# Optimization experiments

Measured on AMD Instinct MI355X. Metric: run time of the kernel, lower is better.

Reference implementation:

```python
import jax, jax.numpy as jnp
import numpy as np

N = 50000
E = 800000
HIGH, LOW, EMB = 128, 32, 64
HID, HEADS, OUT = 32, 8, 8
IN1 = HIGH + EMB  # 192
IN2 = HID * HEADS  # 256
NEG_SLOPE = 0.2


def setup_inputs() -> dict:
    key = jax.random.key(0)
    ks = jax.random.split(key, 12)
    s = lambda k, shape: (jax.random.normal(k, shape, dtype=jnp.float32) * 0.1)
    return {
        "high_dim_features": jax.random.normal(ks[0], (N, HIGH), dtype=jnp.float32),
        "low_dim_features": jax.random.normal(ks[1], (N, LOW), dtype=jnp.float32),
        "edge_index": jax.random.randint(ks[2], (2, E), 0, N, dtype=jnp.int32),
        "W_emb": s(ks[3], (LOW, EMB)),
        "b_emb": jnp.zeros((EMB,), jnp.float32),
        "W1": s(ks[4], (IN1, HEADS * HID)),
        "att_src1": s(ks[5], (HEADS, HID)),
        "att_dst1": s(ks[6], (HEADS, HID)),
        "b1": jnp.zeros((HEADS * HID,), jnp.float32),
        "W2": s(ks[7], (IN2, OUT)),
        "att_src2": s(ks[8], (1, OUT)),
        "att_dst2": s(ks[9], (1, OUT)),
        "b2": jnp.zeros((OUT,), jnp.float32),
    }


def _gat_layer(x, src, dst, W, att_src, att_dst, bias, heads, out_ch, concat):
    # x: [N, F_in]; src/dst: [E'] (self-loops already appended)
    n = x.shape[0]
    h = (x @ W).reshape(n, heads, out_ch)            # [N, H, C]
    a_src = jnp.einsum('nhc,hc->nh', h, att_src)     # [N, H]
    a_dst = jnp.einsum('nhc,hc->nh', h, att_dst)
    alpha = a_src[src] + a_dst[dst]                  # [E', H]
    alpha = jax.nn.leaky_relu(alpha, NEG_SLOPE)
    # segment softmax over incoming edges per destination node
    m = jax.ops.segment_max(alpha, dst, num_segments=n)
    ea = jnp.exp(alpha - m[dst])
    z = jax.ops.segment_sum(ea, dst, num_segments=n)
    alpha = ea / (z[dst] + 1e-16)                    # [E', H]
    msg = h[src] * alpha[:, :, None]                 # [E', H, C]
    out = jax.ops.segment_sum(msg, dst, num_segments=n)  # [N, H, C]
    if concat:
        out = out.reshape(n, heads * out_ch)
    else:
        out = out.mean(axis=1)
    return out + bias


def reference(high_dim_features, low_dim_features, edge_index,
              W_emb, b_emb, W1, att_src1, att_dst1, b1,
              W2, att_src2, att_dst2, b2):
    # embedding + elu, concat
    emb = jax.nn.elu(low_dim_features @ W_emb + b_emb)
    x = jnp.concatenate([high_dim_features, emb], axis=1)  # [N, IN1]
    # add self-loops (PyG default)
    loops = jnp.arange(N, dtype=edge_index.dtype)
    src = jnp.concatenate([edge_index[0], loops])
    dst = jnp.concatenate([edge_index[1], loops])
    x = _gat_layer(x, src, dst, W1, att_src1, att_dst1, b1, HEADS, HID, True)
    x = jax.nn.elu(x)  # dropout: eval mode no-op
    x = _gat_layer(x, src, dst, W2, att_src2, att_dst2, b2, 1, OUT, False)
    return jax.nn.log_softmax(x, axis=1)
```

## Files before the change

kernel.cpp:

```cpp
#include <hip/hip_runtime.h>
#include <hip/hip_bf16.h>

typedef __hip_bfloat16 bf16;
typedef short bf16x8 __attribute__((ext_vector_type(8)));
typedef float f32x4  __attribute__((ext_vector_type(4)));
typedef float f32x2  __attribute__((ext_vector_type(2)));
typedef int   i32x4  __attribute__((ext_vector_type(4)));

#define CHK 2048

__device__ __forceinline__ float bf2f(bf16 v){ return __bfloat162float(v); }
__device__ __forceinline__ bf16  f2bf(float f){ return __float2bfloat16(f); }
__device__ __forceinline__ float lrelu(float a){ return a > 0.f ? a : 0.2f*a; }
__device__ __forceinline__ float bfbits(short s){
    union{unsigned u; float f;} cv; cv.u = ((unsigned)(unsigned short)s) << 16; return cv.f;
}
__device__ __forceinline__ float fbits(int u){ union{int i; float f;} c; c.i = u; return c.f; }
__device__ __forceinline__ short bf16s(float f){ bf16 q = f2bf(f); return *(short*)&q; }
__device__ __forceinline__ float cvtf(const void* p, int i, int isb){
    return isb ? bf2f(((const bf16*)p)[i]) : ((const float*)p)[i];
}
__device__ __forceinline__ short cvts(const void* p, int i, int isb){
    return isb ? ((const short*)p)[i] : bf16s(((const float*)p)[i]);
}
__device__ __forceinline__ bf16x8 load8(const void* base, size_t off, int isb){
    if (isb) return *(const bf16x8*)((const bf16*)base + off);
    const float* f = (const float*)base + off;
    f32x4 v0 = *(const f32x4*)f;
    f32x4 v1 = *(const f32x4*)(f + 4);
    short r[8];
    #pragma unroll
    for (int j = 0; j < 4; j++) r[j]   = bf16s(v0[j]);
    #pragma unroll
    for (int j = 0; j < 4; j++) r[4+j] = bf16s(v1[j]);
    return *(const bf16x8*)r;
}

__device__ __forceinline__ void acc8p(f32x2 acc2[4], float w, bf16x8 v){
    i32x4 iv = *(const i32x4*)&v;
    f32x2 w2 = {w, w};
    #pragma unroll
    for (int k = 0; k < 4; k++){
        int d = iv[k];
        f32x2 hv = {fbits(d << 16), fbits(d & 0xffff0000)};
        acc2[k] += w2 * hv;
    }
}

__global__ __launch_bounds__(256) void k_prep(const unsigned short* __restrict__ raw,
        const void* __restrict__ low,
        const void* __restrict__ Wemb, const void* __restrict__ bemb,
        const void* __restrict__ W1, const void* __restrict__ W2,
        bf16* __restrict__ emb, bf16* __restrict__ Bp, bf16* __restrict__ Bp2,
        const int* __restrict__ dst, int* __restrict__ bucketCnt,
        int* __restrict__ flag, int N, int E, int nEmb, int nPack, int nCnt, int NBUK){
    __shared__ float wem[2048 + 64];
    __shared__ short lows[1024];
    __shared__ int hh[256];
    __shared__ int cnt;
    int t = threadIdx.x;
    int b = blockIdx.x;
    if (b >= nEmb + nPack){
        int cb = b - nEmb - nPack;
        hh[t] = 0;
        __syncthreads();
        for (int i = cb*256 + t; i < E; i += nCnt*256)
            atomicAdd(&hh[((unsigned)dst[i]) >> 8], 1);
        __syncthreads();
        if (t < NBUK && hh[t]) atomicAdd(&bucketCnt[t], hh[t]);
        return;
    }
    {
        unsigned short wd = raw[2*t];
        int ex = (wd >> 7) & 0xFF;
        int ok = (ex >= 90 && ex <= 140) ? 1 : 0;
        if (t == 0) cnt = 0;
        __syncthreads();
        atomicAdd(&cnt, ok);
        __syncthreads();
    }
    int isb = (cnt >= 192) ? 1 : 0;
    if (b == 0 && t == 0) *flag = isb;
    if (b >= nEmb){
        int i = (b - nEmb)*256 + t;
        if (i < 16*6*64*8){
            int j = i & 7;
            int lane = (i >> 3) & 63;
            int r = i >> 9;
            int kt = r % 6, nt = r / 6;
            int k = kt*32 + (lane >> 4)*8 + j;
            int n = nt*16 + (lane & 15);
            *(short*)&Bp[i] = cvts(W1, k*256 + n, isb);
        } else {
            int i2 = i - 16*6*64*8;
            if (i2 >= 8*64*8) return;
            int j = i2 & 7;
            int lane = (i2 >> 3) & 63;
            int kt = i2 >> 9;
            int k = kt*32 + (lane >> 4)*8 + j;
            int n = lane & 15;
            *(short*)&Bp2[i2] = (n < 8) ? cvts(W2, k*8 + n, isb) : (short)0;
        }
        return;
    }
    for (int i = t; i < 2048; i += 256) wem[i] = cvtf(Wemb, i, isb);
    if (t < 64) wem[2048 + t] = cvtf(bemb, t, isb);
    int nl = t >> 3, j8 = (t & 7) * 8;
    for (int tile = 0; tile < 4; tile++){
        int nb0 = b*128 + tile*32;
        __syncthreads();
        int lim = (N - nb0) * 32;
        if (lim > 1024) lim = 1024;
        if (lim < 0) lim = 0;
        for (int i = t; i < 1024; i += 256)
            lows[i] = (i < lim) ? cvts(low, nb0*32 + i, isb) : (short)0;
        __syncthreads();
        float acc[8];
        #pragma unroll
        for (int j = 0; j < 8; j++) acc[j] = wem[2048 + j8 + j];
        for (int k = 0; k < 32; k++){
            float lv = bfbits(lows[nl*32 + k]);
            f32x4 w0 = *(const f32x4*)&wem[k*64 + j8];
            f32x4 w1 = *(const f32x4*)&wem[k*64 + j8 + 4];
            #pragma unroll
            for (int j = 0; j < 4; j++) acc[j]   += lv * w0[j];
            #pragma unroll
            for (int j = 0; j < 4; j++) acc[4+j] += lv * w1[j];
        }
        int n = nb0 + nl;
        if (n < N){
            short ov[8];
            #pragma unroll
            for (int j = 0; j < 8; j++){
                float v = acc[j];
                ov[j] = bf16s(v > 0.f ? v : expm1f(v));
            }
            *(bf16x8*)&emb[(size_t)n*64 + j8] = *(const bf16x8*)ov;
        }
    }
}

__global__ __launch_bounds__(256) void k_bscan(const int* __restrict__ bucketCnt,
        int* __restrict__ bucketPtr, int* __restrict__ bucketCur,
        int* __restrict__ rowptr, int N, int E, int NBUK){
    __shared__ int sd[256];
    int t = threadIdx.x;
    int v = (t < NBUK) ? bucketCnt[t] : 0;
    sd[t] = v;
    __syncthreads();
    #pragma unroll
    for (int off = 1; off < 256; off <<= 1){
        int a = (t >= off) ? sd[t - off] : 0;
        __syncthreads();
        sd[t] += a;
        __syncthreads();
    }
    int excl = sd[t] - v;
    if (t < NBUK){ bucketPtr[t] = excl; bucketCur[t*16] = excl; }
    if (t == 0){ bucketPtr[NBUK] = sd[255]; rowptr[N] = E + N; }
}

__global__ __launch_bounds__(256) void k_sg(
        const int* __restrict__ ei, int* __restrict__ bucketCur, int* __restrict__ pk,
        const void* __restrict__ highv, const bf16* __restrict__ emb,
        const bf16* __restrict__ Bp, const void* __restrict__ attS,
        const void* __restrict__ attD, bf16* __restrict__ h1,
        float* __restrict__ a_s, float* __restrict__ a_d,
        const int* __restrict__ flag, int N, int E, int nScat, int NBUK){
    const int CS  = 17;
    const int RSS = 16*CS + 4;
    __shared__ union SM {
        struct { short Ah[64*128]; short Ae[64*64]; } a;
        struct { float eb[16*276 + 16]; } g;
        struct { unsigned short dstS[CHK]; int hist[4][256]; int cur[4][256]; } s;
    } sm;
    __shared__ float att[512];
    int t = threadIdx.x;
    if ((int)blockIdx.x < nScat){
        int base = blockIdx.x * CHK;
        int cnt = E - base; if (cnt > CHK) cnt = CHK;
        int wv = t >> 6, lane = t & 63;
        #pragma unroll
        for (int w = 0; w < 4; w++) sm.s.hist[w][t] = 0;
        __syncthreads();
        const int* dstp = ei + E + base;
        const int* srcp = ei + base;
        int per = (cnt + 3) >> 2;
        int wb = wv*per, we = wb + per;
        if (we > cnt) we = cnt;
        if (wb > cnt) wb = cnt;
        for (int i = wb + lane; i < we; i += 64){
            int d = dstp[i];
            sm.s.dstS[i] = (unsigned short)d;
            atomicAdd(&sm.s.hist[wv][((unsigned)d) >> 8], 1);
        }
        __syncthreads();
        if (t < NBUK){
            int h0 = sm.s.hist[0][t], h1v = sm.s.hist[1][t];
            int h2 = sm.s.hist[2][t], h3 = sm.s.hist[3][t];
            int c = h0 + h1v + h2 + h3;
            int bs = c ? atomicAdd(&bucketCur[t*16], c) : 0;
            sm.s.cur[0][t] = bs;
            sm.s.cur[1][t] = bs + h0;
            sm.s.cur[2][t] = bs + h0 + h1v;
            sm.s.cur[3][t] = bs + h0 + h1v + h2;
        }
        __syncthreads();
        for (int i = wb + lane; i < we; i += 64){
            int d = sm.s.dstS[i];
            int pos = atomicAdd(&sm.s.cur[wv][d >> 8], 1);
            pk[pos] = ((d & 255) << 24) | srcp[i];
        }
        return;
    }
    int isb = *flag;
    att[t] = cvtf(attS, t, isb);
    att[256 + t] = cvtf(attD, t, isb);
    int w = t >> 6, lane = t & 63;
    int m_lo = lane & 15, quad = lane >> 4;
    int m0 = (blockIdx.x - nScat) * 64;

    #pragma unroll
    for (int ii = 0; ii < 4; ii++){
        int id = t + ii*256;
        int r = id >> 4, c = id & 15;
        int gr = m0 + r; if (gr >= N) gr = N-1;
        bf16x8 v = load8(highv, (size_t)gr*128 + c*8, isb);
        *(bf16x8*)&sm.a.Ah[r*128 + ((c ^ (r & 7)) << 3)] = v;
    }
    #pragma unroll
    for (int ii = 0; ii < 2; ii++){
        int id = t + ii*256;
        int r = id >> 3, c = id & 7;
        int gr = m0 + r; if (gr >= N) gr = N-1;
        bf16x8 v = *(const bf16x8*)&emb[(size_t)gr*64 + c*8];
        *(bf16x8*)&sm.a.Ae[r*64 + ((c ^ (r & 7)) << 3)] = v;
    }
    __syncthreads();

    f32x4 acc[4][4];
    #pragma unroll
    for (int rt = 0; rt < 4; rt++)
        #pragma unroll
        for (int ct = 0; ct < 4; ct++) acc[rt][ct] = (f32x4){0.f,0.f,0.f,0.f};

    int sw = m_lo & 7;
    #pragma unroll 2
    for (int kt = 0; kt < 6; kt++){
        bf16x8 a[4], b[4];
        if (kt < 4){
            int ch = (kt*4 + quad) ^ sw;
            #pragma unroll
            for (int rt = 0; rt < 4; rt++)
                a[rt] = *(const bf16x8*)&sm.a.Ah[(rt*16 + m_lo)*128 + (ch << 3)];
        } else {
            int ch = ((kt-4)*4 + quad) ^ sw;
            #pragma unroll
            for (int rt = 0; rt < 4; rt++)
                a[rt] = *(const bf16x8*)&sm.a.Ae[(rt*16 + m_lo)*64 + (ch << 3)];
        }
        #pragma unroll
        for (int ct = 0; ct < 4; ct++)
            b[ct] = *(const bf16x8*)&Bp[(size_t)(((w*4 + ct)*6 + kt)*64 + lane)*8];
        #pragma unroll
        for (int rt = 0; rt < 4; rt++)
            #pragma unroll
            for (int ct = 0; ct < 4; ct++)
                acc[rt][ct] = __builtin_amdgcn_mfma_f32_16x16x32_bf16(a[rt], b[ct], acc[rt][ct], 0, 0, 0);
    }

    float* eb = sm.g.eb;
    #pragma unroll 1
    for (int rt = 0; rt < 4; rt++){
        __syncthreads();
        #pragma unroll
        for (int ct = 0; ct < 4; ct++)
            #pragma unroll
            for (int reg = 0; reg < 4; reg++)
                eb[(quad*4 + reg)*RSS + (w*4 + ct)*CS + m_lo] = acc[rt][ct][reg];
        __syncthreads();
        int r = t >> 4, cb = t & 15;
        int c0 = cb * 16;
        int m = m0 + rt*16 + r;
        f32x4 v[4];
        #pragma unroll
        for (int p = 0; p < 4; p++) v[p] = *(const f32x4*)&eb[r*RSS + cb*CS + p*4];
        float ps = 0.f, pd = 0.f;
        #pragma unroll
        for (int p = 0; p < 4; p++)
            #pragma unroll
            for (int j = 0; j < 4; j++){
                ps += v[p][j] * att[c0 + p*4 + j];
                pd += v[p][j] * att[256 + c0 + p*4 + j];
            }
        if (m < N){
            short ov[16];
            #pragma unroll
            for (int p = 0; p < 4; p++)
                #pragma unroll
                for (int j = 0; j < 4; j++) ov[p*4+j] = bf16s(v[p][j]);
            *(bf16x8*)&h1[(size_t)m*256 + c0]     = *(const bf16x8*)&ov[0];
            *(bf16x8*)&h1[(size_t)m*256 + c0 + 8] = *(const bf16x8*)&ov[8];
        }
        ps += __shfl_xor(ps, 1);
        pd += __shfl_xor(pd, 1);
        if (((t & 1) == 0) && m < N){
            int hd = cb >> 1;
            a_s[m*8 + hd] = ps;
            a_d[m*8 + hd] = pd;
        }
    }
}

__global__ __launch_bounds__(256) void k_fine(const int* __restrict__ bucketPtr,
        const int* __restrict__ pk, int* __restrict__ rowptr, int* __restrict__ srcs,
        int N){
    __shared__ int hist[4][256];
    __shared__ int cur[4][256];
    __shared__ int sd[256];
    int t = threadIdx.x;
    int wv = t >> 6, lane = t & 63;
    int b = blockIdx.x;
    int d0 = b << 8;
    int nd = N - d0; if (nd > 256) nd = 256; if (nd < 0) nd = 0;
    int ebeg = bucketPtr[b], eend = bucketPtr[b+1];
    int tot = eend - ebeg;
    int per = (tot + 3) >> 2;
    int wb = wv*per, we = wb + per;
    if (we > tot) we = tot;
    if (wb > tot) wb = tot;
    #pragma unroll
    for (int w = 0; w < 4; w++) hist[w][t] = 0;
    __syncthreads();
    for (int i = wb + lane; i < we; i += 64)
        atomicAdd(&hist[wv][((unsigned)pk[ebeg + i]) >> 24], 1);
    __syncthreads();
    int h0 = hist[0][t], h1 = hist[1][t], h2 = hist[2][t], h3 = hist[3][t];
    int selfc = (t < nd) ? 1 : 0;
    int v = selfc + h0 + h1 + h2 + h3;
    sd[t] = v;
    __syncthreads();
    #pragma unroll
    for (int off = 1; off < 256; off <<= 1){
        int a = (t >= off) ? sd[t - off] : 0;
        __syncthreads();
        sd[t] += a;
        __syncthreads();
    }
    int r = ebeg + d0 + sd[t] - v;
    if (t < nd){
        rowptr[d0 + t] = r;
        srcs[r] = d0 + t;
    }
    int c0 = r + selfc;
    cur[0][t] = c0;
    cur[1][t] = c0 + h0;
    cur[2][t] = c0 + h0 + h1;
    cur[3][t] = c0 + h0 + h1 + h2;
    __syncthreads();
    for (int i = wb + lane; i < we; i += 64){
        int p = pk[ebeg + i];
        int pos = atomicAdd(&cur[wv][((unsigned)p) >> 24], 1);
        srcs[pos] = p & 0xFFFFFF;
    }
}

__global__ __launch_bounds__(256) void k_edge1(const int* __restrict__ rowptr,
        const int* __restrict__ srcs, const float* __restrict__ a_s,
        const float* __restrict__ a_d, const bf16* __restrict__ h1,
        const void* __restrict__ b1, bf16* __restrict__ x2,
        const int* __restrict__ flag, int N){
    int t = threadIdx.x;
    int lane = t & 63, wv = t >> 6;
    int n = blockIdx.x*4 + wv;
    if (n >= N) return;
    int beg = rowptr[n];
    int deg = rowptr[n+1] - beg;

    int cl = lane & 31;
    int hb = cl >> 2;
    int half = lane >> 5;
    float adb = a_d[n*8 + hb];

    f32x2 acc2[4];
    #pragma unroll
    for (int k = 0; k < 4; k++) acc2[k] = (f32x2){0.f, 0.f};
    float z = 0.f;

    int e = half;
    if (e + 6 < deg){
        int s0 = srcs[beg + e];
        int s1 = srcs[beg + e + 2];
        int s2 = srcs[beg + e + 4];
        int s3 = srcs[beg + e + 6];
        float a0 = a_s[s0*8 + hb];
        float a1 = a_s[s1*8 + hb];
        float a2 = a_s[s2*8 + hb];
        float a3 = a_s[s3*8 + hb];
        while (true){
            bf16x8 v0 = *(const bf16x8*)&h1[(size_t)s0*256 + cl*8];
            bf16x8 v1 = *(const bf16x8*)&h1[(size_t)s1*256 + cl*8];
            bf16x8 v2 = *(const bf16x8*)&h1[(size_t)s2*256 + cl*8];
            bf16x8 v3 = *(const bf16x8*)&h1[(size_t)s3*256 + cl*8];
            int en = e + 8;
            bool more = (en + 6 < deg);
            int n0, n1, n2, n3;
            float b0, b1, b2, b3;
            if (more){
                n0 = srcs[beg + en];
                n1 = srcs[beg + en + 2];
                n2 = srcs[beg + en + 4];
                n3 = srcs[beg + en + 6];
                b0 = a_s[n0*8 + hb];
                b1 = a_s[n1*8 + hb];
                b2 = a_s[n2*8 + hb];
                b3 = a_s[n3*8 + hb];
            }
            float w0 = __expf(fminf(lrelu(a0 + adb), 80.f));
            float w1 = __expf(fminf(lrelu(a1 + adb), 80.f));
            float w2 = __expf(fminf(lrelu(a2 + adb), 80.f));
            float w3 = __expf(fminf(lrelu(a3 + adb), 80.f));
            z += (w0 + w1) + (w2 + w3);
            acc8p(acc2, w0, v0);
            acc8p(acc2, w1, v1);
            acc8p(acc2, w2, v2);
            acc8p(acc2, w3, v3);
            e = en;
            if (!more) break;
            s0 = n0; s1 = n1; s2 = n2; s3 = n3;
            a0 = b0; a1 = b1; a2 = b2; a3 = b3;
        }
    }
    for (; e < deg; e += 2){
        int s = srcs[beg + e];
        float w = __expf(fminf(lrelu(a_s[s*8 + hb] + adb), 80.f));
        bf16x8 hv = *(const bf16x8*)&h1[(size_t)s*256 + cl*8];
        z += w;
        acc8p(acc2, w, hv);
    }
    float acc[8];
    #pragma unroll
    for (int k = 0; k < 4; k++){ acc[2*k] = acc2[k][0]; acc[2*k+1] = acc2[k][1]; }
    #pragma unroll
    for (int j = 0; j < 8; j++) acc[j] += __shfl_xor(acc[j], 32);
    z += __shfl_xor(z, 32);
    float rz = 1.f / (z + 1e-16f);

    if (half == 0){
        int isb = *flag;
        bf16x8 bv = load8(b1, cl*8, isb);
        short ov[8];
        #pragma unroll
        for (int j = 0; j < 8; j++){
            float v = acc[j] * rz + bfbits(bv[j]);
            ov[j] = bf16s(v > 0.f ? v : expm1f(v));
        }
        *(bf16x8*)&x2[(size_t)n*256 + cl*8] = *(const bf16x8*)ov;
    }
}

__global__ __launch_bounds__(256) void k_gemm2(const bf16* __restrict__ x2,
        const bf16* __restrict__ Bp2, const void* __restrict__ attS,
        const void* __restrict__ attD, float* __restrict__ h2,
        float* __restrict__ a2s, float* __restrict__ a2d,
        const int* __restrict__ flag, int N){
    int t = threadIdx.x;
    int isb = *flag;
    int w = t >> 6, lane = t & 63;
    int m_lo = lane & 15, quad = lane >> 4;
    int m0 = blockIdx.x*64 + w*16;
    int mr = m0 + m_lo; if (mr >= N) mr = N-1;
    f32x4 acc = (f32x4){0.f,0.f,0.f,0.f};
    #pragma unroll
    for (int kt = 0; kt < 8; kt++){
        bf16x8 a = *(const bf16x8*)&x2[(size_t)mr*256 + kt*32 + quad*8];
        bf16x8 b = *(const bf16x8*)&Bp2[(size_t)(kt*64 + lane)*8];
        acc = __builtin_amdgcn_mfma_f32_16x16x32_bf16(a, b, acc, 0, 0, 0);
    }
    float s2 = (m_lo < 8) ? cvtf(attS, m_lo, isb) : 0.f;
    float d2 = (m_lo < 8) ? cvtf(attD, m_lo, isb) : 0.f;
    #pragma unroll
    for (int reg = 0; reg < 4; reg++){
        int m = m0 + quad*4 + reg;
        float val = acc[reg];
        float ps = val * s2, pd = val * d2;
        ps += __shfl_xor(ps, 1); ps += __shfl_xor(ps, 2);
        ps += __shfl_xor(ps, 4); ps += __shfl_xor(ps, 8);
        pd += __shfl_xor(pd, 1); pd += __shfl_xor(pd, 2);
        pd += __shfl_xor(pd, 4); pd += __shfl_xor(pd, 8);
        if (m < N){
            if (m_lo < 8) h2[(size_t)m*8 + m_lo] = val;
            if (m_lo == 0){ a2s[m] = ps; a2d[m] = pd; }
        }
    }
}

__global__ __launch_bounds__(256) void k_edge2(const int* __restrict__ rowptr,
        const int* __restrict__ srcs, const float* __restrict__ a2s,
        const float* __restrict__ a2d, const float* __restrict__ h2,
        const void* __restrict__ b2, void* __restrict__ outv,
        const int* __restrict__ flag, int N){
    int t = threadIdx.x;
    int lane = t & 63, wv = t >> 6;
    int n = blockIdx.x*4 + wv;
    if (n >= N) return;
    int beg = rowptr[n];
    int deg = rowptr[n+1] - beg;
    float adh = a2d[n];
    int ep = lane >> 3, c = lane & 7;
    float acc = 0.f, z = 0.f;
    int e = ep;
    if (e + 8 < deg){
        int s0 = srcs[beg + e];
        int s1 = srcs[beg + e + 8];
        float a0 = a2s[s0], a1 = a2s[s1];
        float g0 = h2[(size_t)s0*8 + c], g1 = h2[(size_t)s1*8 + c];
        while (true){
            int en = e + 16;
            bool more = (en + 8 < deg);
            int n0, n1; float b0, b1, f0, f1;
            if (more){
                n0 = srcs[beg + en];
                n1 = srcs[beg + en + 8];
                b0 = a2s[n0]; b1 = a2s[n1];
                f0 = h2[(size_t)n0*8 + c]; f1 = h2[(size_t)n1*8 + c];
            }
            float w0 = __expf(fminf(lrelu(a0 + adh), 80.f));
            float w1 = __expf(fminf(lrelu(a1 + adh), 80.f));
            z += w0 + w1;
            acc += w0 * g0 + w1 * g1;
            e = en;
            if (!more) break;
            s0 = n0; s1 = n1; a0 = b0; a1 = b1; g0 = f0; g1 = f1;
        }
    }
    for (; e < deg; e += 8){
        int s = srcs[beg + e];
        float w = __expf(fminf(lrelu(a2s[s] + adh), 80.f));
        z += w;
        acc += w * h2[(size_t)s*8 + c];
    }
    acc += __shfl_xor(acc, 8);
    acc += __shfl_xor(acc, 16);
    acc += __shfl_xor(acc, 32);
    z += __shfl_xor(z, 8);
    z += __shfl_xor(z, 16);
    z += __shfl_xor(z, 32);
    int isb = *flag;
    float val = acc / (z + 1e-16f) + cvtf(b2, c, isb);
    float mx = val;
    mx = fmaxf(mx, __shfl_xor(mx, 1));
    mx = fmaxf(mx, __shfl_xor(mx, 2));
    mx = fmaxf(mx, __shfl_xor(mx, 4));
    float se = __expf(val - mx);
    se += __shfl_xor(se, 1); se += __shfl_xor(se, 2); se += __shfl_xor(se, 4);
    float r = val - mx - __logf(se);
    if (lane < 8){
        if (isb) ((bf16*)outv)[(size_t)n*8 + c] = f2bf(r);
        else     ((float*)outv)[(size_t)n*8 + c] = r;
    }
}

extern "C" void kernel_launch(void* const* d_in, const int* in_sizes, int n_in,
                              void* d_out, int out_size, void* d_ws, size_t ws_size,
                              hipStream_t stream) {
    const int* ei = (const int*)d_in[2];
    const int N = in_sizes[0] / 128;
    const int E = in_sizes[2] / 2;
    const int ET = E + N;
    const int NBUK = (N + 255) >> 8;

    char* p = (char*)d_ws;
    auto alloc = [&](size_t bytes) -> void* {
        char* r = p;
        p += (bytes + 255) & ~(size_t)255;
        return (void*)r;
    };
    int*   flag      = (int*)  alloc(256);
    int*   bucketCnt = (int*)  alloc((size_t)NBUK*4);
    int*   bucketPtr = (int*)  alloc((size_t)(NBUK+1)*4);
    int*   bucketCur = (int*)  alloc((size_t)NBUK*16*4);
    int*   rowptr    = (int*)  alloc((size_t)(N+1)*4);
    int*   srcs      = (int*)  alloc((size_t)ET*4);
    int*   pk        = (int*)  alloc((size_t)E*4);
    bf16*  Bp        = (bf16*) alloc((size_t)192*256*2);
    bf16*  Bp2       = (bf16*) alloc((size_t)8*64*8*2);
    bf16*  emb       = (bf16*) alloc((size_t)N*64*2);
    bf16*  h1        = (bf16*) alloc((size_t)N*256*2);
    float* a_s       = (float*)alloc((size_t)N*8*4);
    float* a_d       = (float*)alloc((size_t)N*8*4);
    bf16*  x2        = (bf16*) alloc((size_t)N*256*2);
    float* h2        = (float*)alloc((size_t)N*8*4);
    float* a2s       = (float*)alloc((size_t)N*4);
    float* a2d       = (float*)alloc((size_t)N*4);

    hipMemsetAsync(bucketCnt, 0, (size_t)NBUK*4, stream);
    {
        int nEmb  = (N + 127)/128;
        int nPack = (16*6*64*8 + 8*64*8 + 255)/256;
        int nCnt  = 256;
        k_prep<<<nEmb + nPack + nCnt, 256, 0, stream>>>(
                (const unsigned short*)d_in[0], d_in[1], d_in[3], d_in[4],
                d_in[5], d_in[9], emb, Bp, Bp2,
                ei + E, bucketCnt, flag, N, E, nEmb, nPack, nCnt, NBUK);
    }
    k_bscan<<<1, 256, 0, stream>>>(bucketCnt, bucketPtr, bucketCur, rowptr, N, E, NBUK);
    {
        int nG = (N + 63)/64;
        int nScat = (E + CHK - 1)/CHK;
        k_sg<<<nScat + nG, 256, 0, stream>>>(ei, bucketCur, pk,
                d_in[0], emb, Bp, d_in[6], d_in[7], h1, a_s, a_d, flag, N, E, nScat, NBUK);
    }
    k_fine<<<NBUK, 256, 0, stream>>>(bucketPtr, pk, rowptr, srcs, N);
    k_edge1<<<(N + 3)/4, 256, 0, stream>>>(rowptr, srcs, a_s, a_d, h1, d_in[8], x2, flag, N);
    k_gemm2<<<(N + 63)/64, 256, 0, stream>>>(x2, Bp2, d_in[10], d_in[11], h2, a2s, a2d, flag, N);
    k_edge2<<<(N + 3)/4, 256, 0, stream>>>(rowptr, srcs, a2s, a2d, h2, d_in[12], d_out, flag, N);
}
```

Before: 297.8 us.

## Precompute GAT layer-1 attention weights and normalizers in a separate kernel

Adds a k_wgt kernel that computes the exponentiated attention weights for every edge and head, stores them in a new per-edge buffer, and stores the inverse softmax normalizer per node and head. k_edge1 then reads these weights instead of gathering a_s and evaluating exp, and drops its own normalizer reduction. The aim is to take the dependent random gathers and transcendental math out of the bandwidth-bound aggregation loop. The cost is an extra kernel launch and writing and re-reading about 850K×8 floats of weights.

```diff
diff --git a/kernel.cpp b/kernel.cpp
--- a/kernel.cpp
+++ b/kernel.cpp
@@ -365,9 +365,33 @@
     }
 }
 
+__global__ __launch_bounds__(256) void k_wgt(const int* __restrict__ rowptr,
+        const int* __restrict__ srcs, const float* __restrict__ a_s,
+        const float* __restrict__ a_d, float* __restrict__ wts,
+        float* __restrict__ zinv, int N){
+    int t = threadIdx.x;
+    int lane = t & 63, wv = t >> 6;
+    int n = blockIdx.x*4 + wv;
+    if (n >= N) return;
+    int beg = rowptr[n], end = rowptr[n+1];
+    int ep = lane >> 3, c = lane & 7;
+    float ad = a_d[n*8 + c];
+    float z = 0.f;
+    for (int e = beg + ep; e < end; e += 8){
+        int s = srcs[e];
+        float w = __expf(fminf(lrelu(a_s[s*8 + c] + ad), 80.f));
+        z += w;
+        wts[(size_t)e*8 + c] = w;
+    }
+    z += __shfl_xor(z, 8);
+    z += __shfl_xor(z, 16);
+    z += __shfl_xor(z, 32);
+    if (lane < 8) zinv[n*8 + c] = 1.f / (z + 1e-16f);
+}
+
 __global__ __launch_bounds__(256) void k_edge1(const int* __restrict__ rowptr,
-        const int* __restrict__ srcs, const float* __restrict__ a_s,
-        const float* __restrict__ a_d, const bf16* __restrict__ h1,
+        const int* __restrict__ srcs, const float* __restrict__ wts,
+        const float* __restrict__ zinv, const bf16* __restrict__ h1,
         const void* __restrict__ b1, bf16* __restrict__ x2,
         const int* __restrict__ flag, int N){
     int t = threadIdx.x;
@@ -380,12 +404,12 @@
     int cl = lane & 31;
     int hb = cl >> 2;
     int half = lane >> 5;
-    float adb = a_d[n*8 + hb];
+    float rz = zinv[n*8 + hb];
+    const float* wp = wts + (size_t)beg*8 + hb;
 
     f32x2 acc2[4];
     #pragma unroll
     for (int k = 0; k < 4; k++) acc2[k] = (f32x2){0.f, 0.f};
-    float z = 0.f;
 
     int e = half;
     if (e + 6 < deg){
@@ -393,34 +417,24 @@
         int s1 = srcs[beg + e + 2];
         int s2 = srcs[beg + e + 4];
         int s3 = srcs[beg + e + 6];
-        float a0 = a_s[s0*8 + hb];
-        float a1 = a_s[s1*8 + hb];
-        float a2 = a_s[s2*8 + hb];
-        float a3 = a_s[s3*8 + hb];
         while (true){
             bf16x8 v0 = *(const bf16x8*)&h1[(size_t)s0*256 + cl*8];
             bf16x8 v1 = *(const bf16x8*)&h1[(size_t)s1*256 + cl*8];
             bf16x8 v2 = *(const bf16x8*)&h1[(size_t)s2*256 + cl*8];
             bf16x8 v3 = *(const bf16x8*)&h1[(size_t)s3*256 + cl*8];
+            float w0 = wp[(size_t)e*8];
+            float w1 = wp[(size_t)(e+2)*8];
+            float w2 = wp[(size_t)(e+4)*8];
+            float w3 = wp[(size_t)(e+6)*8];
             int en = e + 8;
             bool more = (en + 6 < deg);
             int n0, n1, n2, n3;
-            float b0, b1, b2, b3;
             if (more){
                 n0 = srcs[beg + en];
                 n1 = srcs[beg + en + 2];
                 n2 = srcs[beg + en + 4];
                 n3 = srcs[beg + en + 6];
-                b0 = a_s[n0*8 + hb];
-                b1 = a_s[n1*8 + hb];
-                b2 = a_s[n2*8 + hb];
-                b3 = a_s[n3*8 + hb];
             }
-            float w0 = __expf(fminf(lrelu(a0 + adb), 80.f));
-            float w1 = __expf(fminf(lrelu(a1 + adb), 80.f));
-            float w2 = __expf(fminf(lrelu(a2 + adb), 80.f));
-            float w3 = __expf(fminf(lrelu(a3 + adb), 80.f));
-            z += (w0 + w1) + (w2 + w3);
             acc8p(acc2, w0, v0);
             acc8p(acc2, w1, v1);
             acc8p(acc2, w2, v2);
@@ -428,14 +442,12 @@
             e = en;
             if (!more) break;
             s0 = n0; s1 = n1; s2 = n2; s3 = n3;
-            a0 = b0; a1 = b1; a2 = b2; a3 = b3;
         }
     }
     for (; e < deg; e += 2){
         int s = srcs[beg + e];
-        float w = __expf(fminf(lrelu(a_s[s*8 + hb] + adb), 80.f));
+        float w = wp[(size_t)e*8];
         bf16x8 hv = *(const bf16x8*)&h1[(size_t)s*256 + cl*8];
-        z += w;
         acc8p(acc2, w, hv);
     }
     float acc[8];
@@ -443,8 +455,6 @@
     for (int k = 0; k < 4; k++){ acc[2*k] = acc2[k][0]; acc[2*k+1] = acc2[k][1]; }
     #pragma unroll
     for (int j = 0; j < 8; j++) acc[j] += __shfl_xor(acc[j], 32);
-    z += __shfl_xor(z, 32);
-    float rz = 1.f / (z + 1e-16f);
 
     if (half == 0){
         int isb = *flag;
@@ -589,6 +599,8 @@
     bf16*  h1        = (bf16*) alloc((size_t)N*256*2);
     float* a_s       = (float*)alloc((size_t)N*8*4);
     float* a_d       = (float*)alloc((size_t)N*8*4);
+    float* wts       = (float*)alloc((size_t)ET*8*4);
+    float* zinv      = (float*)alloc((size_t)N*8*4);
     bf16*  x2        = (bf16*) alloc((size_t)N*256*2);
     float* h2        = (float*)alloc((size_t)N*8*4);
     float* a2s       = (float*)alloc((size_t)N*4);
@@ -612,7 +624,8 @@
                 d_in[0], emb, Bp, d_in[6], d_in[7], h1, a_s, a_d, flag, N, E, nScat, NBUK);
     }
     k_fine<<<NBUK, 256, 0, stream>>>(bucketPtr, pk, rowptr, srcs, N);
-    k_edge1<<<(N + 3)/4, 256, 0, stream>>>(rowptr, srcs, a_s, a_d, h1, d_in[8], x2, flag, N);
+    k_wgt<<<(N + 3)/4, 256, 0, stream>>>(rowptr, srcs, a_s, a_d, wts, zinv, N);
+    k_edge1<<<(N + 3)/4, 256, 0, stream>>>(rowptr, srcs, wts, zinv, h1, d_in[8], x2, flag, N);
     k_gemm2<<<(N + 63)/64, 256, 0, stream>>>(x2, Bp2, d_in[10], d_in[11], h2, a2s, a2d, flag, N);
     k_edge2<<<(N + 3)/4, 256, 0, stream>>>(rowptr, srcs, a2s, a2d, h2, d_in[12], d_out, flag, N);
 }
```

Result: slower. 310.9 us (+4.4%).
